# Kernel optimization log

Hardware: AMD Instinct MI355X
Metric: run time of the kernel (lower is better)

Reference implementation:

```python
import jax, jax.numpy as jnp
import numpy as np

B, S, E, H = 4, 2048, 1024, 16
D = E // H  # head dim = 64


def setup_inputs() -> dict:
    key = jax.random.key(0)
    ks = jax.random.split(key, 5)
    scale = 0.02
    return {
        "x": jax.random.normal(ks[0], (B, S, E), dtype=jnp.float32),
        "Wa_w": jax.random.normal(ks[1], (3 * E, E), dtype=jnp.float32) * scale,
        "Wa_b": jax.random.normal(ks[2], (3 * E,), dtype=jnp.float32) * scale,
        "Wo_w": jax.random.normal(ks[3], (E, E), dtype=jnp.float32) * scale,
        "Wo_b": jax.random.normal(ks[4], (E,), dtype=jnp.float32) * scale,
    }


def reference(x, Wa_w, Wa_b, Wo_w, Wo_b):
    b, s, e = x.shape
    # Fused QKV projection (torch Linear: x @ W^T + b)
    qkv = jnp.einsum("bse,fe->bsf", x, Wa_w) + Wa_b  # [B,S,3E]
    q, k, v = jnp.split(qkv, 3, axis=-1)
    # [B,S,E] -> [B,H,S,D]
    def heads(t):
        return t.reshape(b, s, H, D).transpose(0, 2, 1, 3)
    q, k, v = heads(q), heads(k), heads(v)
    # Causal attention with explicit score matrix (as in the original)
    scores = jnp.einsum("bhqd,bhkd->bhqk", q, k) / jnp.sqrt(jnp.float32(D))
    causal = jnp.tril(jnp.ones((s, s), dtype=bool))
    scores = jnp.where(causal, scores, -jnp.inf)
    attn = jax.nn.softmax(scores, axis=-1)  # dropout p=0 -> identity
    out = jnp.einsum("bhqk,bhkd->bhqd", attn, v)  # [B,H,S,D]
    out = out.transpose(0, 2, 1, 3).reshape(b, s, e)
    return jnp.einsum("bse,fe->bsf", out, Wo_w) + Wo_b
```

## Files before the change

kernel.cpp:

```cpp
#include <hip/hip_runtime.h>
#include <hip/hip_bf16.h>
#include <cstdint>

typedef __bf16 bf16_t;
typedef __attribute__((ext_vector_type(8))) __bf16 bf16x8;
typedef __attribute__((ext_vector_type(4))) __bf16 bf16x4;
typedef __attribute__((ext_vector_type(4))) float f32x4;

#define B_ 4
#define S_ 2048
#define E_ 1024
#define H_ 16
#define D_ 64

#define QSCALE 0.18033688011112042f

__global__ void cvt_f32_to_bf16(const float* __restrict__ in, bf16_t* __restrict__ out, int n4) {
    int i = blockIdx.x * blockDim.x + threadIdx.x;
    int stride = gridDim.x * blockDim.x;
    for (; i < n4; i += stride) {
        f32x4 v = reinterpret_cast<const f32x4*>(in)[i];
        bf16x4 o;
        o.x = (bf16_t)v.x; o.y = (bf16_t)v.y; o.z = (bf16_t)v.z; o.w = (bf16_t)v.w;
        reinterpret_cast<bf16x4*>(out)[i] = o;
    }
}

__device__ __forceinline__ void gload_lds16(const bf16_t* g, bf16_t* l) {
    __builtin_amdgcn_global_load_lds((const __attribute__((address_space(1))) void*)g,
                                     (__attribute__((address_space(3))) void*)l, 16, 0, 0);
}

__device__ __forceinline__ void wait_vm4() { asm volatile("s_waitcnt vmcnt(4)" ::: "memory"); }
__device__ __forceinline__ void wait_vm0() { asm volatile("s_waitcnt vmcnt(0)" ::: "memory"); }

template <int MODE>
__launch_bounds__(256, 3)
__global__ void gemm_pipe(const bf16_t* __restrict__ A, const bf16_t* __restrict__ Bm,
                          const float* __restrict__ bias,
                          int M, int N, int NG,
                          bf16_t* __restrict__ Qg, bf16_t* __restrict__ Kg,
                          bf16_t* __restrict__ Vtg, float* __restrict__ Outf) {
    constexpr int K = 1024, BK = 32, NKT = K / BK;
    constexpr int BM = 128, BN = 128;
    __shared__ __align__(16) bf16_t As[3][BM * BK];
    __shared__ __align__(16) bf16_t Bs[3][BN * BK];

    const int xcd = blockIdx.x & 7;
    const int u = blockIdx.x >> 3;
    const int grp = 8 * NG;
    const int g = u / grp, r2 = u % grp;
    const int ntl = r2 / 8, mtl = r2 & 7;
    const int mt = xcd * 8 + mtl;
    const int nt = g * NG + ntl;
    const int m0 = mt * BM, n0 = nt * BN;

    const int t = threadIdx.x;
    const int lane = t & 63;
    const int wid = t >> 6;
    const int wr = wid >> 1, wc = wid & 1;
    const int lr = lane & 15, lg = lane >> 4;

    auto mkSrc = [&](const bf16_t* base, int c, int row0) {
        const int line = c >> 3, chg = (c & 7) ^ (line & 7);
        return base + (int64_t)(row0 + 2 * line + (chg >> 2)) * K + (chg & 3) * 8;
    };
    const bf16_t* aSrc0 = mkSrc(A, t, m0);
    const bf16_t* aSrc1 = mkSrc(A, t + 256, m0);
    const bf16_t* bSrc0 = mkSrc(Bm, t, n0);
    const bf16_t* bSrc1 = mkSrc(Bm, t + 256, n0);

    auto stageT = [&](int kt, int buf) {
        gload_lds16(aSrc0 + kt * BK, &As[buf][t * 8]);
        gload_lds16(aSrc1 + kt * BK, &As[buf][(t + 256) * 8]);
        gload_lds16(bSrc0 + kt * BK, &Bs[buf][t * 8]);
        gload_lds16(bSrc1 + kt * BK, &Bs[buf][(t + 256) * 8]);
    };

    auto fragOff = [](int row, int kc) -> int {
        const int line = row >> 1;
        const int ch = ((row & 1) << 2) | kc;
        return line * 64 + ((ch ^ (line & 7)) << 3);
    };

    f32x4 acc[4][4] = {};

    stageT(0, 0);
    stageT(1, 1);

    int bufc = 0, bufs = 2;
    for (int kt = 0; kt < NKT; ++kt) {
        if (kt < NKT - 1) wait_vm4(); else wait_vm0();
        __builtin_amdgcn_s_barrier();
        __builtin_amdgcn_sched_barrier(0);

        if (kt + 2 < NKT) stageT(kt + 2, bufs);

        bf16x8 bfr[4], afr[4];
#pragma unroll
        for (int j = 0; j < 4; ++j)
            bfr[j] = *(const bf16x8*)&Bs[bufc][fragOff(wc * 64 + j * 16 + lr, lg)];
#pragma unroll
        for (int i = 0; i < 4; ++i)
            afr[i] = *(const bf16x8*)&As[bufc][fragOff(wr * 64 + i * 16 + lr, lg)];

        __builtin_amdgcn_s_setprio(1);
#pragma unroll
        for (int i = 0; i < 4; ++i)
#pragma unroll
            for (int j = 0; j < 4; ++j)
                acc[i][j] = __builtin_amdgcn_mfma_f32_16x16x32_bf16(afr[i], bfr[j], acc[i][j], 0, 0, 0);
        __builtin_amdgcn_s_setprio(0);

        bufc = (bufc == 2) ? 0 : bufc + 1;
        bufs = (bufs == 2) ? 0 : bufs + 1;
    }

    if (MODE == 0) {
        const int which = n0 >> 10;
#pragma unroll
        for (int j = 0; j < 4; ++j) {
            const int f = n0 + wc * 64 + j * 16 + lr;
            const float bv = bias[f];
            const int fe = f - which * E_;
            const int h = fe >> 6, d = fe & 63;
#pragma unroll
            for (int i = 0; i < 4; ++i) {
#pragma unroll
                for (int r = 0; r < 4; ++r) {
                    const int m = m0 + wr * 64 + i * 16 + lg * 4 + r;
                    const int b = m >> 11, si = m & (S_ - 1);
                    const float v = acc[i][j][r] + bv;
                    if (which == 0)
                        Qg[(((int64_t)(b * H_ + h)) * S_ + si) * D_ + d] = (bf16_t)(v * QSCALE);
                    else if (which == 1)
                        Kg[(((int64_t)(b * H_ + h)) * S_ + si) * D_ + d] = (bf16_t)v;
                    else
                        Vtg[(((int64_t)(b * H_ + h)) * D_ + d) * S_ + si] = (bf16_t)v;
                }
            }
        }
    } else {
#pragma unroll
        for (int j = 0; j < 4; ++j) {
            const int f = n0 + wc * 64 + j * 16 + lr;
            const float bv = bias[f];
#pragma unroll
            for (int i = 0; i < 4; ++i) {
#pragma unroll
                for (int r = 0; r < 4; ++r) {
                    const int m = m0 + wr * 64 + i * 16 + lg * 4 + r;
                    Outf[(int64_t)m * N + f] = acc[i][j][r] + bv;
                }
            }
        }
    }
}

__launch_bounds__(256, 4)
__global__ void attn_causal(const bf16_t* __restrict__ Qg, const bf16_t* __restrict__ Kg,
                            const bf16_t* __restrict__ Vtg, bf16_t* __restrict__ Og) {
    __shared__ __align__(16) bf16_t Ks[2][64 * 64];
    __shared__ __align__(16) bf16_t Vs[2][64 * 64];
    __shared__ __align__(16) bf16_t P_lds[4][16 * 64];

    const int bid = blockIdx.x;
    const int xcd = bid & 7, j = bid >> 3;
    const int bh = (j >> 4) * 8 + xcd;
    const int i = j & 15;
    const int qtA = i, qtB = 31 - i;

    const int t = threadIdx.x, lane = t & 63, w = t >> 6;
    const int lr = lane & 15, lg = lane >> 4;
    const int q0A = qtA * 64 + w * 16;
    const int q0B = qtB * 64 + w * 16;

    const bf16_t* Qb = Qg + (int64_t)bh * S_ * D_;
    const bf16_t* Kb = Kg + (int64_t)bh * S_ * D_;
    const bf16_t* Vb = Vtg + (int64_t)bh * D_ * S_;

    const int srow = t >> 3;
    const int scol_sw = (t & 7) ^ (srow & 7);

    auto stageK = [&](int buf, int kv0) {
        const bf16_t* base = Kb + (kv0 + srow) * D_ + scol_sw * 8;
        gload_lds16(base, &Ks[buf][t * 8]);
        gload_lds16(base + 32 * D_, &Ks[buf][t * 8 + 2048]);
    };
    auto stageV = [&](int buf, int kv0) {
        const bf16_t* base = Vb + srow * S_ + kv0 + scol_sw * 8;
        gload_lds16(base, &Vs[buf][t * 8]);
        gload_lds16(base + 32 * S_, &Vs[buf][t * 8 + 2048]);
    };

    auto psw = [](int row, int col) {
        return row * 64 + ((((col >> 3) ^ (row & 7)) << 3) | (col & 7));
    };

    bf16x8 qfA[2], qfB[2];
#pragma unroll
    for (int kk = 0; kk < 2; ++kk) {
        qfA[kk] = *(const bf16x8*)&Qb[(q0A + lr) * D_ + kk * 32 + lg * 8];
        qfB[kk] = *(const bf16x8*)&Qb[(q0B + lr) * D_ + kk * 32 + lg * 8];
    }

    bf16x8 ones;
#pragma unroll
    for (int e = 0; e < 8; ++e) ones[e] = (bf16_t)1.0f;

    f32x4 oA[4] = {}, oB[4] = {};
    f32x4 lA = {}, lB = {};

    int cur = 0;
    stageK(0, 0);
    stageV(0, 0);
    __syncthreads();

    for (int tkv = 0; tkv <= qtB; ++tkv) {
        const int kv0 = tkv * 64;
        if (tkv < qtB) { stageK(cur ^ 1, kv0 + 64); stageV(cur ^ 1, kv0 + 64); }

        auto process = [&](int q0, const bf16x8* qf, f32x4* o, f32x4& accl, bf16_t* Pw) {
            f32x4 sc[4] = {};
            __builtin_amdgcn_s_setprio(1);
#pragma unroll
            for (int nj = 0; nj < 4; ++nj) {
                if (kv0 + nj * 16 <= q0 + 15) {
                    const int krow = nj * 16 + lr;
#pragma unroll
                    for (int kk = 0; kk < 2; ++kk) {
                        bf16x8 kfr = *(const bf16x8*)&Ks[cur][krow * 64 + (((kk * 4 + lg) ^ (krow & 7)) * 8)];
                        sc[nj] = __builtin_amdgcn_mfma_f32_16x16x32_bf16(qf[kk], kfr, sc[nj], 0, 0, 0);
                    }
                }
            }
            __builtin_amdgcn_s_setprio(0);

            if (kv0 + 64 > q0) {
#pragma unroll
                for (int nj = 0; nj < 4; ++nj) {
                    const int col = kv0 + nj * 16 + lr;
#pragma unroll
                    for (int r = 0; r < 4; ++r) {
                        const int rowg = q0 + lg * 4 + r;
                        if (col > rowg) sc[nj][r] = -1e30f;
                    }
                }
            }

#pragma unroll
            for (int nj = 0; nj < 4; ++nj)
#pragma unroll
                for (int r = 0; r < 4; ++r)
                    Pw[psw(lg * 4 + r, nj * 16 + lr)] = (bf16_t)__builtin_amdgcn_exp2f(sc[nj][r]);
            asm volatile("s_waitcnt lgkmcnt(0)" ::: "memory");
            __builtin_amdgcn_sched_barrier(0);

            __builtin_amdgcn_s_setprio(1);
#pragma unroll
            for (int kk = 0; kk < 2; ++kk) {
                bf16x8 pa = *(const bf16x8*)&Pw[psw(lr, kk * 32 + lg * 8)];
                accl = __builtin_amdgcn_mfma_f32_16x16x32_bf16(pa, ones, accl, 0, 0, 0);
#pragma unroll
                for (int nd = 0; nd < 4; ++nd) {
                    const int vrow = nd * 16 + lr;
                    bf16x8 vf = *(const bf16x8*)&Vs[cur][vrow * 64 + (((kk * 4 + lg) ^ (vrow & 7)) * 8)];
                    o[nd] = __builtin_amdgcn_mfma_f32_16x16x32_bf16(pa, vf, o[nd], 0, 0, 0);
                }
            }
            __builtin_amdgcn_s_setprio(0);
        };

        process(q0B, qfB, oB, lB, &P_lds[w][0]);
        if (tkv <= qtA) process(q0A, qfA, oA, lA, &P_lds[w][0]);

        __syncthreads();
        cur ^= 1;
    }

    const int b = bh >> 4, h = bh & 15;
#pragma unroll
    for (int r = 0; r < 4; ++r) {
        const float rlA = 1.0f / lA[r];
        const float rlB = 1.0f / lB[r];
        const int rA = q0A + lg * 4 + r;
        const int rB = q0B + lg * 4 + r;
#pragma unroll
        for (int nd = 0; nd < 4; ++nd) {
            Og[((int64_t)(b * S_ + rA)) * E_ + h * D_ + nd * 16 + lr] = (bf16_t)(oA[nd][r] * rlA);
            Og[((int64_t)(b * S_ + rB)) * E_ + h * D_ + nd * 16 + lr] = (bf16_t)(oB[nd][r] * rlB);
        }
    }
}

extern "C" void kernel_launch(void* const* d_in, const int* in_sizes, int n_in,
                              void* d_out, int out_size, void* d_ws, size_t ws_size,
                              hipStream_t stream) {
    const float* x    = (const float*)d_in[0];
    const float* Wa_w = (const float*)d_in[1];
    const float* Wa_b = (const float*)d_in[2];
    const float* Wo_w = (const float*)d_in[3];
    const float* Wo_b = (const float*)d_in[4];
    float* out = (float*)d_out;

    const size_t M = (size_t)B_ * S_;
    char* ws = (char*)d_ws;
    bf16_t* xb  = (bf16_t*)ws; ws += M * E_ * 2;
    bf16_t* wab = (bf16_t*)ws; ws += (size_t)3 * E_ * E_ * 2;
    bf16_t* wob = (bf16_t*)ws; ws += (size_t)E_ * E_ * 2;
    bf16_t* Qg  = (bf16_t*)ws; ws += M * E_ * 2;
    bf16_t* Kg  = (bf16_t*)ws; ws += M * E_ * 2;
    bf16_t* Vtg = (bf16_t*)ws; ws += M * E_ * 2;
    bf16_t* Og  = (bf16_t*)ws; ws += M * E_ * 2;

    cvt_f32_to_bf16<<<2048, 256, 0, stream>>>(x, xb, (int)(M * E_ / 4));
    cvt_f32_to_bf16<<<768, 256, 0, stream>>>(Wa_w, wab, 3 * E_ * E_ / 4);
    cvt_f32_to_bf16<<<256, 256, 0, stream>>>(Wo_w, wob, E_ * E_ / 4);

    gemm_pipe<0><<<1536, 256, 0, stream>>>(
        xb, wab, Wa_b, 8192, 3072, 12, Qg, Kg, Vtg, nullptr);

    attn_causal<<<B_ * H_ * 16, 256, 0, stream>>>(Qg, Kg, Vtg, Og);

    gemm_pipe<1><<<512, 256, 0, stream>>>(
        Og, wob, Wo_b, 8192, 1024, 8, nullptr, nullptr, nullptr, out);
}
```

Baseline: 189.6 us.

## Merge conversion kernels, drop MFMA priority boosts, restructure GEMM epilogue

Fuses the three fp32-to-bf16 conversion launches into one grid-stride kernel over all three tensors, removing two launches and their tails. It removes the s_setprio raise/lower around the MFMA block in the GEMM loop. The epilogue now hoists the four bias loads and reorders the loops so each lane computes one row base address and writes four columns, with the head index computed once per block. The fused conversion adds per-element branching, and dropping setprio may change how waves interleave loads and math.

```diff
diff --git a/kernel.cpp b/kernel.cpp
--- a/kernel.cpp
+++ b/kernel.cpp
@@ -15,14 +15,24 @@
 
 #define QSCALE 0.18033688011112042f
 
-__global__ void cvt_f32_to_bf16(const float* __restrict__ in, bf16_t* __restrict__ out, int n4) {
+__global__ void cvt_all(const float* __restrict__ x, const float* __restrict__ wa,
+                        const float* __restrict__ wo,
+                        bf16_t* __restrict__ xb, bf16_t* __restrict__ wab,
+                        bf16_t* __restrict__ wob) {
+    constexpr int N1 = (B_ * S_ * E_) / 4;
+    constexpr int N2 = (3 * E_ * E_) / 4;
+    constexpr int N3 = (E_ * E_) / 4;
     int i = blockIdx.x * blockDim.x + threadIdx.x;
     int stride = gridDim.x * blockDim.x;
-    for (; i < n4; i += stride) {
-        f32x4 v = reinterpret_cast<const f32x4*>(in)[i];
+    for (; i < N1 + N2 + N3; i += stride) {
+        const float* src; bf16_t* dst; int k;
+        if (i < N1) { src = x; dst = xb; k = i; }
+        else if (i < N1 + N2) { src = wa; dst = wab; k = i - N1; }
+        else { src = wo; dst = wob; k = i - N1 - N2; }
+        f32x4 v = reinterpret_cast<const f32x4*>(src)[k];
         bf16x4 o;
         o.x = (bf16_t)v.x; o.y = (bf16_t)v.y; o.z = (bf16_t)v.z; o.w = (bf16_t)v.w;
-        reinterpret_cast<bf16x4*>(out)[i] = o;
+        reinterpret_cast<bf16x4*>(dst)[k] = o;
     }
 }
 
@@ -104,54 +114,57 @@
         for (int i = 0; i < 4; ++i)
             afr[i] = *(const bf16x8*)&As[bufc][fragOff(wr * 64 + i * 16 + lr, lg)];
 
-        __builtin_amdgcn_s_setprio(1);
 #pragma unroll
         for (int i = 0; i < 4; ++i)
 #pragma unroll
             for (int j = 0; j < 4; ++j)
                 acc[i][j] = __builtin_amdgcn_mfma_f32_16x16x32_bf16(afr[i], bfr[j], acc[i][j], 0, 0, 0);
-        __builtin_amdgcn_s_setprio(0);
 
         bufc = (bufc == 2) ? 0 : bufc + 1;
         bufs = (bufs == 2) ? 0 : bufs + 1;
     }
 
+    float bv[4];
+#pragma unroll
+    for (int j = 0; j < 4; ++j) bv[j] = bias[n0 + wc * 64 + j * 16 + lr];
+
     if (MODE == 0) {
         const int which = n0 >> 10;
-#pragma unroll
-        for (int j = 0; j < 4; ++j) {
-            const int f = n0 + wc * 64 + j * 16 + lr;
-            const float bv = bias[f];
-            const int fe = f - which * E_;
-            const int h = fe >> 6, d = fe & 63;
-#pragma unroll
-            for (int i = 0; i < 4; ++i) {
-#pragma unroll
-                for (int r = 0; r < 4; ++r) {
-                    const int m = m0 + wr * 64 + i * 16 + lg * 4 + r;
-                    const int b = m >> 11, si = m & (S_ - 1);
-                    const float v = acc[i][j][r] + bv;
-                    if (which == 0)
-                        Qg[(((int64_t)(b * H_ + h)) * S_ + si) * D_ + d] = (bf16_t)(v * QSCALE);
-                    else if (which == 1)
-                        Kg[(((int64_t)(b * H_ + h)) * S_ + si) * D_ + d] = (bf16_t)v;
-                    else
-                        Vtg[(((int64_t)(b * H_ + h)) * D_ + d) * S_ + si] = (bf16_t)v;
+        const int h = (((n0 & 1023) + wc * 64) >> 6);
+#pragma unroll
+        for (int i = 0; i < 4; ++i) {
+#pragma unroll
+            for (int r = 0; r < 4; ++r) {
+                const int m = m0 + wr * 64 + i * 16 + lg * 4 + r;
+                const int b = m >> 11, si = m & (S_ - 1);
+                if (which == 0) {
+                    bf16_t* p = &Qg[(((int64_t)(b * H_ + h)) * S_ + si) * D_ + lr];
+#pragma unroll
+                    for (int j = 0; j < 4; ++j)
+                        p[j * 16] = (bf16_t)((acc[i][j][r] + bv[j]) * QSCALE);
+                } else if (which == 1) {
+                    bf16_t* p = &Kg[(((int64_t)(b * H_ + h)) * S_ + si) * D_ + lr];
+#pragma unroll
+                    for (int j = 0; j < 4; ++j)
+                        p[j * 16] = (bf16_t)(acc[i][j][r] + bv[j]);
+                } else {
+                    bf16_t* p = &Vtg[(((int64_t)(b * H_ + h)) * D_ + lr) * S_ + si];
+#pragma unroll
+                    for (int j = 0; j < 4; ++j)
+                        p[(int64_t)(j * 16) * S_] = (bf16_t)(acc[i][j][r] + bv[j]);
                 }
             }
         }
     } else {
 #pragma unroll
-        for (int j = 0; j < 4; ++j) {
-            const int f = n0 + wc * 64 + j * 16 + lr;
-            const float bv = bias[f];
-#pragma unroll
-            for (int i = 0; i < 4; ++i) {
-#pragma unroll
-                for (int r = 0; r < 4; ++r) {
-                    const int m = m0 + wr * 64 + i * 16 + lg * 4 + r;
-                    Outf[(int64_t)m * N + f] = acc[i][j][r] + bv;
-                }
+        for (int i = 0; i < 4; ++i) {
+#pragma unroll
+            for (int r = 0; r < 4; ++r) {
+                const int m = m0 + wr * 64 + i * 16 + lg * 4 + r;
+                float* p = &Outf[(int64_t)m * N + n0 + wc * 64 + lr];
+#pragma unroll
+                for (int j = 0; j < 4; ++j)
+                    p[j * 16] = acc[i][j][r] + bv[j];
             }
         }
     }
@@ -313,9 +326,7 @@
     bf16_t* Vtg = (bf16_t*)ws; ws += M * E_ * 2;
     bf16_t* Og  = (bf16_t*)ws; ws += M * E_ * 2;
 
-    cvt_f32_to_bf16<<<2048, 256, 0, stream>>>(x, xb, (int)(M * E_ / 4));
-    cvt_f32_to_bf16<<<768, 256, 0, stream>>>(Wa_w, wab, 3 * E_ * E_ / 4);
-    cvt_f32_to_bf16<<<256, 256, 0, stream>>>(Wo_w, wob, E_ * E_ / 4);
+    cvt_all<<<2048, 256, 0, stream>>>(x, Wa_w, Wo_w, xb, wab, wob);
 
     gemm_pipe<0><<<1536, 256, 0, stream>>>(
         xb, wab, Wa_b, 8192, 3072, 12, Qg, Kg, Vtg, nullptr);
```

Result: faster. 180.2 us (-4.9%).
